# Kernel tuning notes

Hardware: AMD Instinct MI355X
Metric: run time of the kernel (lower is better)

Reference implementation:

```python
import jax, jax.numpy as jnp
import numpy as np

# Expert output sizes per answer type: yes/no, number, other (VQA v2)
SIZES = [2, 482, 3129]
MAX_ANS = max(SIZES)  # 3129, padded output width
D_IN = 1024
D_HID = 1000
BATCH = 16384
N_TYPES = len(SIZES)


def setup_inputs() -> dict:
    key = jax.random.key(0)
    ks = jax.random.split(key, 2 + 4 * N_TYPES)
    inp = {
        "hidden_states": jax.random.normal(ks[0], (BATCH, D_IN), dtype=jnp.float32),
        "question_type_output": jax.random.normal(ks[1], (BATCH, N_TYPES), dtype=jnp.float32),
    }
    # Learned params for each expert MLP: Linear(1024->1000), Tanh, Linear(1000->n_e)
    for e, n_out in enumerate(SIZES):
        k1, k2, k3, k4 = ks[2 + 4 * e], ks[3 + 4 * e], ks[4 + 4 * e], ks[5 + 4 * e]
        inp[f"w1_{e}"] = jax.random.normal(k1, (D_IN, D_HID), dtype=jnp.float32) * 0.02
        inp[f"b1_{e}"] = jax.random.normal(k2, (D_HID,), dtype=jnp.float32) * 0.02
        inp[f"w2_{e}"] = jax.random.normal(k3, (D_HID, n_out), dtype=jnp.float32) * 0.02
        inp[f"b2_{e}"] = jax.random.normal(k4, (n_out,), dtype=jnp.float32) * 0.02
    return inp


def _expert(x, w1, b1, w2, b2):
    # Linear -> Dropout(eval: identity) -> Tanh -> Linear
    return jnp.tanh(x @ w1 + b1) @ w2 + b2


def reference(hidden_states, question_type_output,
              w1_0, b1_0, w2_0, b2_0,
              w1_1, b1_1, w2_1, b2_1,
              w1_2, b1_2, w2_2, b2_2):
    params = [(w1_0, b1_0, w2_0, b2_0),
              (w1_1, b1_1, w2_1, b2_1),
              (w1_2, b1_2, w2_2, b2_2)]
    # Route each sample to the expert of its argmax question type.
    pred = jnp.argmax(question_type_output, axis=1)  # [B] int
    out = jnp.zeros((hidden_states.shape[0], MAX_ANS), dtype=hidden_states.dtype)
    # Small fixed loop over N_TYPES experts (structurally distinct weights);
    # each expert runs batched over all samples, then a mask selects routed rows.
    for e, (w1, b1, w2, b2) in enumerate(params):
        o = _expert(hidden_states, w1, b1, w2, b2)          # [B, n_e]
        o = jnp.pad(o, ((0, 0), (0, MAX_ANS - o.shape[1])))  # zero-pad to [B, MAX]
        out = jnp.where((pred == e)[:, None], o, out)
    return out
```

## Files before the change

### kernel.cpp

```cpp
#include <hip/hip_runtime.h>

typedef __attribute__((ext_vector_type(8))) __bf16 bf16x8;
typedef __attribute__((ext_vector_type(4))) float f32x4;

constexpr int BATCH = 16384;
constexpr int DIN   = 1024;
constexpr int DHID  = 1000;
constexpr int MAXA  = 3129;
constexpr int MBMAX = 131;

constexpr size_t SZ_AP  = (size_t)MBMAX * 32 * 8192;
constexpr size_t SZ_HP  = SZ_AP;
constexpr size_t SZ_W1P = 3 * 8 * 32 * 8192;
constexpr size_t SZ_W2P = 30 * 32 * 8192;
constexpr size_t WS_HP  = 0;
constexpr size_t WS_W1P = WS_HP + SZ_HP;
constexpr size_t WS_W2P = WS_W1P + SZ_W1P;
constexpr size_t WS_CNT = WS_W2P + SZ_W2P;
constexpr size_t WS_IDX = WS_CNT + 64;
constexpr size_t WS_AP  = WS_IDX + 3 * BATCH * 4;
constexpr size_t WS_NEED = WS_AP + SZ_AP;

constexpr int PA_BLK = 2096;
constexpr int PW1_BLK = 1536;
constexpr int PW2_BLK = 1920;

__device__ __forceinline__ ushort f2bf(float f) {
    return __builtin_bit_cast(ushort, (__bf16)f);
}

__device__ __forceinline__ void gload16(const void* g, void* l) {
    __builtin_amdgcn_global_load_lds((const __attribute__((address_space(1))) void*)g,
                                     (__attribute__((address_space(3))) void*)l, 16, 0, 0);
}

__global__ void zero_k(int* __restrict__ c) {
    if (threadIdx.x < 16) c[threadIdx.x] = 0;
}

__global__ void route_k(const float* __restrict__ qt, int* __restrict__ counts,
                        int* __restrict__ idx) {
    int i = blockIdx.x * 256 + threadIdx.x;
    if (i >= BATCH) return;
    float a = qt[3 * i], b = qt[3 * i + 1], c = qt[3 * i + 2];
    int p = 0; float m = a;
    if (b > m) { m = b; p = 1; }
    if (c > m) { m = c; p = 2; }
    int pos = atomicAdd(&counts[p], 1);
    idx[p * BATCH + pos] = i;
}

__global__ void pack_all_k(const float* __restrict__ hs,
                           const float* __restrict__ w1_0, const float* __restrict__ w1_1,
                           const float* __restrict__ w1_2,
                           const float* __restrict__ w2_0, const float* __restrict__ w2_1,
                           const float* __restrict__ w2_2,
                           const int* __restrict__ counts, const int* __restrict__ idx,
                           ushort* __restrict__ Ap, ushort* __restrict__ W1p,
                           ushort* __restrict__ W2p) {
    const int b = blockIdx.x, tid = threadIdx.x;
    if (b < PA_BLK) {
        const int g = b * 256 + tid;
        const int m = g & 127, kt = (g >> 7) & 31, mb = g >> 12;
        const int c0 = counts[0], c1 = counts[1], c2 = counts[2];
        const int n0 = (c0 + 127) >> 7, n1 = (c1 + 127) >> 7, n2 = (c2 + 127) >> 7;
        if (mb >= n0 + n1 + n2) return;
        int e = 0, lm = mb, cnt = c0;
        if (lm >= n0) { lm -= n0; e = 1; cnt = c1; }
        if (e == 1 && lm >= n1) { lm -= n1; e = 2; cnt = c2; }
        int ri = lm * 128 + m; if (ri >= cnt) ri = cnt - 1;
        const float* row = hs + (size_t)idx[e * BATCH + ri] * DIN + kt * 32;
        ushort* dst = Ap + (size_t)(mb * 32 + kt) * 4096 + m * 8;
#pragma unroll
        for (int kc = 0; kc < 4; kc++) {
            float4 f0 = *reinterpret_cast<const float4*>(row + kc * 8);
            float4 f1 = *reinterpret_cast<const float4*>(row + kc * 8 + 4);
            union { ushort u[8]; int4 v; } p;
            p.u[0] = f2bf(f0.x); p.u[1] = f2bf(f0.y); p.u[2] = f2bf(f0.z); p.u[3] = f2bf(f0.w);
            p.u[4] = f2bf(f1.x); p.u[5] = f2bf(f1.y); p.u[6] = f2bf(f1.z); p.u[7] = f2bf(f1.w);
            *reinterpret_cast<int4*>(dst + kc * 1024) = p.v;
        }
    } else if (b < PA_BLK + PW1_BLK) {
        const int g = (b - PA_BLK) * 256 + tid;
        const int n = g & 127, kc = (g >> 7) & 3, kt = (g >> 9) & 31, nb = (g >> 14) & 7, e = g >> 17;
        const float* W = e == 0 ? w1_0 : e == 1 ? w1_1 : w1_2;
        const int nn = nb * 128 + n;
        union { ushort u[8]; int4 v; } p;
#pragma unroll
        for (int j = 0; j < 8; j++) {
            int k = kt * 32 + kc * 8 + j;
            float f = (nn < DHID) ? W[(size_t)k * DHID + nn] : 0.f;
            p.u[j] = f2bf(f);
        }
        *reinterpret_cast<int4*>(W1p + ((size_t)((e * 8 + nb) * 32 + kt)) * 4096 + (kc * 128 + n) * 8) = p.v;
    } else {
        const int g = (b - PA_BLK - PW1_BLK) * 256 + tid;
        const int n = g & 127, kc = (g >> 7) & 3, kt = (g >> 9) & 31, t = g >> 14;
        const int e = (t < 1) ? 0 : (t < 5) ? 1 : 2;
        const int nb = t - (e == 0 ? 0 : e == 1 ? 1 : 5);
        const int ne = e == 0 ? 2 : e == 1 ? 482 : MAXA;
        const float* W = e == 0 ? w2_0 : e == 1 ? w2_1 : w2_2;
        const int nn = nb * 128 + n;
        union { ushort u[8]; int4 v; } p;
#pragma unroll
        for (int j = 0; j < 8; j++) {
            int k = kt * 32 + kc * 8 + j;
            float f = (k < DHID && nn < ne) ? W[(size_t)k * ne + nn] : 0.f;
            p.u[j] = f2bf(f);
        }
        *reinterpret_cast<int4*>(W2p + ((size_t)(t * 32 + kt)) * 4096 + (kc * 128 + n) * 8) = p.v;
    }
}

#define STAGE(BUFO, KT)                                                         \
    {                                                                           \
        const char* as_ = Ag + (size_t)(KT) * 8192 + tid * 16;                  \
        char* ad_ = lds + (BUFO) + w * 1024;                                    \
        gload16(as_, ad_);                                                      \
        gload16(as_ + 4096, ad_ + 4096);                                        \
        const char* bs_ = Bg + (size_t)(KT) * 8192 + tid * 16;                  \
        gload16(bs_, ad_ + 8192);                                               \
        gload16(bs_ + 4096, ad_ + 12288);                                       \
    }

#define KLOOP()                                                                 \
    f32x4 acc[4][4] = {};                                                       \
    STAGE(0, 0)                                                                 \
    STAGE(16384, 1)                                                             \
    {                                                                           \
        int cur = 0;                                                            \
        for (int kt = 0; kt < 32; ++kt) {                                       \
            if (kt < 31) asm volatile("s_waitcnt vmcnt(4)" ::: "memory");       \
            else         asm volatile("s_waitcnt vmcnt(0)" ::: "memory");       \
            asm volatile("s_barrier" ::: "memory");                             \
            if (kt + 2 < 32) {                                                  \
                int nx = cur + 2; if (nx >= 3) nx -= 3;                         \
                STAGE(nx * 16384, kt + 2)                                       \
            }                                                                   \
            const char* base = lds + cur * 16384;                               \
            bf16x8 af[4], bfr[4];                                               \
            _Pragma("unroll")                                                   \
            for (int mi = 0; mi < 4; mi++)                                      \
                af[mi] = *reinterpret_cast<const bf16x8*>(                      \
                    base + kq4 * 2048 + (wm * 64 + mi * 16 + l15) * 16);        \
            _Pragma("unroll")                                                   \
            for (int ni = 0; ni < 4; ni++)                                      \
                bfr[ni] = *reinterpret_cast<const bf16x8*>(                     \
                    base + 8192 + kq4 * 2048 + (wn * 64 + ni * 16 + l15) * 16); \
            __builtin_amdgcn_s_setprio(1);                                      \
            _Pragma("unroll")                                                   \
            for (int mi = 0; mi < 4; mi++)                                      \
                _Pragma("unroll")                                               \
                for (int ni = 0; ni < 4; ni++)                                  \
                    acc[mi][ni] = __builtin_amdgcn_mfma_f32_16x16x32_bf16(      \
                        af[mi], bfr[ni], acc[mi][ni], 0, 0, 0);                 \
            __builtin_amdgcn_s_setprio(0);                                      \
            cur = cur + 1; if (cur == 3) cur = 0;                               \
        }                                                                       \
    }                                                                           \
    asm volatile("s_barrier" ::: "memory");

__global__ __launch_bounds__(256, 3)
void gemm1_k(const char* __restrict__ ApB, const char* __restrict__ W1pB,
             const float* __restrict__ b1_0, const float* __restrict__ b1_1,
             const float* __restrict__ b1_2,
             const int* __restrict__ counts, int* __restrict__ wq,
             char* __restrict__ HpB) {
    __shared__ __align__(16) char lds[49152];
    __shared__ int s_t;
    const int c0 = counts[0], c1 = counts[1], c2 = counts[2];
    const int n0 = (c0 + 127) >> 7, n1 = (c1 + 127) >> 7, n2 = (c2 + 127) >> 7;
    const int T = (n0 + n1 + n2) * 8;

    const int tid = threadIdx.x;
    const int lane = tid & 63, w = tid >> 6, wm = w >> 1, wn = w & 1;
    const int l15 = lane & 15, kq4 = lane >> 4;

    for (;;) {
        if (tid == 0) s_t = atomicAdd(wq, 1);
        __syncthreads();
        const int t = s_t;
        if (t >= T) break;

        const int mbG = t >> 3, nbk = t & 7;
        int e = 0, lm = mbG;
        if (lm >= n0) { lm -= n0; e = 1; }
        if (e == 1 && lm >= n1) { lm -= n1; e = 2; }
        const float* bias = e == 0 ? b1_0 : e == 1 ? b1_1 : b1_2;
        const char* Ag = ApB + (size_t)mbG * (32 * 8192);
        const char* Bg = W1pB + (size_t)((e * 8 + nbk) * 32) * 8192;

        KLOOP()

        ushort* img = (ushort*)lds;
#pragma unroll
        for (int mi = 0; mi < 4; mi++) {
            const int rb = wm * 64 + mi * 16 + kq4 * 4;
#pragma unroll
            for (int ni = 0; ni < 4; ni++) {
                const int nl = wn * 64 + ni * 16 + l15;
                const int ng = nbk * 128 + nl;
                const bool live = ng < DHID;
                const float bv = live ? bias[ng] : 0.f;
                const int ua = ((nl >> 5) * 4096 + ((nl >> 3) & 3) * 1024 + (nl & 6)) & ~1;
#pragma unroll
                for (int rg = 0; rg < 4; rg++) {
                    float vv = live ? tanhf(acc[mi][ni][rg] + bv) : 0.f;
                    float vo = __shfl_xor(vv, 1);
                    ushort lo = (l15 & 1) ? f2bf(vo) : f2bf(vv);
                    ushort hi = (l15 & 1) ? f2bf(vv) : f2bf(vo);
                    *reinterpret_cast<uint*>(img + ua + (rb + rg) * 8) =
                        (uint)lo | ((uint)hi << 16);
                }
            }
        }
        asm volatile("s_barrier" ::: "memory");
        char* hdst = HpB + ((size_t)mbG * 32 + nbk * 4) * 8192;
#pragma unroll
        for (int i2 = 0; i2 < 8; i2++) {
            const int s = tid + i2 * 256;
            *reinterpret_cast<int4*>(hdst + s * 16) =
                *reinterpret_cast<const int4*>(lds + s * 16);
        }
        asm volatile("s_barrier" ::: "memory");
    }
}

__global__ __launch_bounds__(256, 3)
void gemm2_k(const char* __restrict__ HpB, const char* __restrict__ W2pB,
             const float* __restrict__ b2_0, const float* __restrict__ b2_1,
             const float* __restrict__ b2_2,
             const int* __restrict__ counts, const int* __restrict__ idx,
             int* __restrict__ wq, int do_zero, float* __restrict__ Out) {
    __shared__ __align__(16) char lds[49152];
    __shared__ int s_t;
    const int c0 = counts[0], c1 = counts[1], c2 = counts[2];
    int nb[3]  = {(c0 + 127) >> 7, (c1 + 127) >> 7, (c2 + 127) >> 7};
    int cc[3]  = {c0, c1, c2};
    const int nbn[3]  = {1, 4, 25};
    const int nz[3]   = {24, 21, 0};
    const int zst[3]  = {128, 512, 0};
    const int toff[3] = {0, 1, 5};
    const int nel[3]  = {2, 482, MAXA};
    const int Tc = nb[0] * 1 + nb[1] * 4 + nb[2] * 25;
    const int Tz = do_zero ? (nb[0] * 24 + nb[1] * 21) : 0;
    const int T = Tc + Tz;

    const int tid = threadIdx.x;
    const int lane = tid & 63, w = tid >> 6, wm = w >> 1, wn = w & 1;
    const int l15 = lane & 15, kq4 = lane >> 4;

    for (;;) {
        if (tid == 0) s_t = atomicAdd(wq, 1);
        __syncthreads();
        const int t = s_t;
        if (t >= T) break;

        if (t < Tc) {
            int e = 0, r = t, mbG = 0;
            while (e < 2 && r >= nb[e] * nbn[e]) { r -= nb[e] * nbn[e]; mbG += nb[e]; ++e; }
            const int lm = r / nbn[e], nbk = r - lm * nbn[e];
            mbG += lm;
            const int cnt = cc[e], ne = nel[e];
            const float* bias = e == 0 ? b2_0 : e == 1 ? b2_1 : b2_2;
            const char* Ag = HpB + (size_t)mbG * (32 * 8192);
            const char* Bg = W2pB + (size_t)((toff[e] + nbk) * 32) * 8192;

            KLOOP()

            const int m0 = lm * 128;
            float* bf32 = (float*)lds;
            const int* ip = idx + e * BATCH;
#pragma unroll
            for (int h = 0; h < 2; h++) {
                if (wm == h) {
#pragma unroll
                    for (int mi = 0; mi < 4; mi++) {
                        const int rl = mi * 16 + kq4 * 4;
#pragma unroll
                        for (int ni = 0; ni < 4; ni++) {
                            const int nl = wn * 64 + ni * 16 + l15;
                            const int ncol = nbk * 128 + nl;
                            const bool live = ncol < ne;
                            const float bv = live ? bias[ncol] : 0.f;
#pragma unroll
                            for (int rg = 0; rg < 4; rg++)
                                bf32[(rl + rg) * 132 + nl] =
                                    live ? (acc[mi][ni][rg] + bv) : 0.f;
                        }
                    }
                }
                asm volatile("s_barrier" ::: "memory");
#pragma unroll
                for (int i2 = 0; i2 < 8; i2++) {
                    const int s = tid + i2 * 256;
                    const int rr = s >> 5, c4 = s & 31;
                    const int mrow = m0 + h * 64 + rr;
                    const int ncol0 = nbk * 128 + c4 * 4;
                    if (mrow < cnt && ncol0 < ne) {
                        const int orow = ip[mrow];
                        float4 val = *reinterpret_cast<const float4*>(bf32 + rr * 132 + c4 * 4);
                        float* op = Out + (size_t)orow * MAXA + ncol0;
                        if (ncol0 + 3 < MAXA) {
                            *reinterpret_cast<float4*>(op) = val;
                        } else {
                            if (ncol0 + 0 < MAXA) op[0] = val.x;
                            if (ncol0 + 1 < MAXA) op[1] = val.y;
                            if (ncol0 + 2 < MAXA) op[2] = val.z;
                            if (ncol0 + 3 < MAXA) op[3] = val.w;
                        }
                    }
                }
                asm volatile("s_barrier" ::: "memory");
            }
        } else {
            int e = 0, r = t - Tc;
            while (e < 2 && r >= nb[e] * nz[e]) { r -= nb[e] * nz[e]; ++e; }
            const int lm = r / nz[e], zc = r - lm * nz[e];
            const int cnt = cc[e];
            const int col0 = zst[e] + zc * 128;
            const int width = (MAXA - col0 < 128) ? (MAXA - col0) : 128;
            const int m0 = lm * 128;
            const int nrow = (cnt - m0 < 128) ? (cnt - m0) : 128;
            const int* rowp = idx + e * BATCH + m0;
            const float4 z4 = {0.f, 0.f, 0.f, 0.f};
            if (width == 128) {
                for (int s = tid; s < (nrow << 5); s += 256) {
                    const int rl = s >> 5, c4 = s & 31;
                    *reinterpret_cast<float4*>(Out + (size_t)rowp[rl] * MAXA + col0 + c4 * 4) = z4;
                }
            } else {
                const int f4 = width >> 2;
                for (int s = tid; s < nrow * f4; s += 256) {
                    const int rl = s / f4, c4 = s - rl * f4;
                    *reinterpret_cast<float4*>(Out + (size_t)rowp[rl] * MAXA + col0 + c4 * 4) = z4;
                }
                const int rem = width & 3;
                for (int s = tid; s < nrow * rem; s += 256) {
                    const int rl = s / rem, j = s - rl * rem;
                    Out[(size_t)rowp[rl] * MAXA + col0 + f4 * 4 + j] = 0.f;
                }
            }
            __syncthreads();
        }
    }
}

extern "C" void kernel_launch(void* const* d_in, const int* in_sizes, int n_in,
                              void* d_out, int out_size, void* d_ws, size_t ws_size,
                              hipStream_t stream) {
    const float* hs = (const float*)d_in[0];
    const float* qt = (const float*)d_in[1];
    const float* w1_0 = (const float*)d_in[2],  *b1_0 = (const float*)d_in[3];
    const float* w2_0 = (const float*)d_in[4],  *b2_0 = (const float*)d_in[5];
    const float* w1_1 = (const float*)d_in[6],  *b1_1 = (const float*)d_in[7];
    const float* w2_1 = (const float*)d_in[8],  *b2_1 = (const float*)d_in[9];
    const float* w1_2 = (const float*)d_in[10], *b1_2 = (const float*)d_in[11];
    const float* w2_2 = (const float*)d_in[12], *b2_2 = (const float*)d_in[13];

    char* ws = (char*)d_ws;
    ushort* Hp  = (ushort*)(ws + WS_HP);
    ushort* W1p = (ushort*)(ws + WS_W1P);
    ushort* W2p = (ushort*)(ws + WS_W2P);
    int* counts = (int*)(ws + WS_CNT);
    int* idx    = (int*)(ws + WS_IDX);
    const int fallback = (ws_size >= WS_NEED) ? 0 : 1;
    ushort* Ap = fallback ? (ushort*)((char*)d_out + ((size_t)out_size * 4 - SZ_AP))
                          : (ushort*)(ws + WS_AP);
    float* Out = (float*)d_out;

    zero_k<<<1, 64, 0, stream>>>(counts);
    route_k<<<64, 256, 0, stream>>>(qt, counts, idx);
    pack_all_k<<<PA_BLK + PW1_BLK + PW2_BLK, 256, 0, stream>>>(
        hs, w1_0, w1_1, w1_2, w2_0, w2_1, w2_2, counts, idx, Ap, W1p, W2p);
    gemm1_k<<<768, 256, 0, stream>>>((const char*)Ap, (const char*)W1p,
                                     b1_0, b1_1, b1_2, counts, counts + 8, (char*)Hp);
    gemm2_k<<<768, 256, 0, stream>>>((const char*)Hp, (const char*)W2p,
                                     b2_0, b2_1, b2_2, counts, idx, counts + 12,
                                     fallback, Out);
}
```

Baseline: 300.7 us.

## Widen GEMM tiles to 128x256 with repacked weights and wider epilogue

Both GEMM kernels move from 128x128 output tiles to 128x256 tiles. Each wave now holds a 4x8 MFMA accumulator block, so every loaded A fragment is reused across twice as many B columns. Weight packing is reorganised into 256-wide column tiles, LDS per block grows to 72KB, and occupancy drops from 3 to 2 blocks per CU with a smaller persistent grid. The aim is to cut LDS and global traffic per FLOP, at the cost of more register pressure, lower occupancy, and more wasted padded work on the narrow experts.

```diff
diff --git a/kernel.cpp b/kernel.cpp
--- a/kernel.cpp
+++ b/kernel.cpp
@@ -11,19 +11,19 @@
 
 constexpr size_t SZ_AP  = (size_t)MBMAX * 32 * 8192;
 constexpr size_t SZ_HP  = SZ_AP;
-constexpr size_t SZ_W1P = 3 * 8 * 32 * 8192;
-constexpr size_t SZ_W2P = 30 * 32 * 8192;
+constexpr size_t SZ_W1P = (size_t)12 * 32 * 16384;
+constexpr size_t SZ_W2P = (size_t)16 * 32 * 16384;
 constexpr size_t WS_HP  = 0;
 constexpr size_t WS_W1P = WS_HP + SZ_HP;
 constexpr size_t WS_W2P = WS_W1P + SZ_W1P;
 constexpr size_t WS_CNT = WS_W2P + SZ_W2P;
-constexpr size_t WS_IDX = WS_CNT + 64;
-constexpr size_t WS_AP  = WS_IDX + 3 * BATCH * 4;
+constexpr size_t WS_IDX = WS_CNT + 1024;
+constexpr size_t WS_AP  = WS_IDX + (size_t)3 * BATCH * 4;
 constexpr size_t WS_NEED = WS_AP + SZ_AP;
 
-constexpr int PA_BLK = 2096;
-constexpr int PW1_BLK = 1536;
-constexpr int PW2_BLK = 1920;
+constexpr int PA_BLK  = 2096;
+constexpr int PW1_BLK = 384;
+constexpr int PW2_BLK = 512;
 
 __device__ __forceinline__ ushort f2bf(float f) {
     return __builtin_bit_cast(ushort, (__bf16)f);
@@ -34,9 +34,7 @@
                                      (__attribute__((address_space(3))) void*)l, 16, 0, 0);
 }
 
-__global__ void zero_k(int* __restrict__ c) {
-    if (threadIdx.x < 16) c[threadIdx.x] = 0;
-}
+__global__ void zero_k(int* __restrict__ c) { if (threadIdx.x < 16) c[threadIdx.x] = 0; }
 
 __global__ void route_k(const float* __restrict__ qt, int* __restrict__ counts,
                         int* __restrict__ idx) {
@@ -81,77 +79,89 @@
             *reinterpret_cast<int4*>(dst + kc * 1024) = p.v;
         }
     } else if (b < PA_BLK + PW1_BLK) {
-        const int g = (b - PA_BLK) * 256 + tid;
-        const int n = g & 127, kc = (g >> 7) & 3, kt = (g >> 9) & 31, nb = (g >> 14) & 7, e = g >> 17;
+        const int bb = b - PA_BLK;
+        const int kt = bb & 31, tile = bb >> 5;
+        const int e = tile >> 2, nbk = tile & 3;
         const float* W = e == 0 ? w1_0 : e == 1 ? w1_1 : w1_2;
-        const int nn = nb * 128 + n;
-        union { ushort u[8]; int4 v; } p;
-#pragma unroll
-        for (int j = 0; j < 8; j++) {
-            int k = kt * 32 + kc * 8 + j;
-            float f = (nn < DHID) ? W[(size_t)k * DHID + nn] : 0.f;
-            p.u[j] = f2bf(f);
-        }
-        *reinterpret_cast<int4*>(W1p + ((size_t)((e * 8 + nb) * 32 + kt)) * 4096 + (kc * 128 + n) * 8) = p.v;
+        const int n = nbk * 256 + tid;
+        ushort* dst = W1p + (size_t)(tile * 32 + kt) * 8192 + tid * 8;
+#pragma unroll
+        for (int kc = 0; kc < 4; kc++) {
+            union { ushort u[8]; int4 v; } p;
+#pragma unroll
+            for (int j = 0; j < 8; j++) {
+                int k = kt * 32 + kc * 8 + j;
+                float f = (n < DHID) ? W[(size_t)k * DHID + n] : 0.f;
+                p.u[j] = f2bf(f);
+            }
+            *reinterpret_cast<int4*>(dst + kc * 2048) = p.v;
+        }
     } else {
-        const int g = (b - PA_BLK - PW1_BLK) * 256 + tid;
-        const int n = g & 127, kc = (g >> 7) & 3, kt = (g >> 9) & 31, t = g >> 14;
-        const int e = (t < 1) ? 0 : (t < 5) ? 1 : 2;
-        const int nb = t - (e == 0 ? 0 : e == 1 ? 1 : 5);
+        const int bb = b - PA_BLK - PW1_BLK;
+        const int kt = bb & 31, t = bb >> 5;
+        const int e = (t < 1) ? 0 : (t < 3) ? 1 : 2;
+        const int nb = t - (e == 0 ? 0 : e == 1 ? 1 : 3);
         const int ne = e == 0 ? 2 : e == 1 ? 482 : MAXA;
         const float* W = e == 0 ? w2_0 : e == 1 ? w2_1 : w2_2;
-        const int nn = nb * 128 + n;
-        union { ushort u[8]; int4 v; } p;
-#pragma unroll
-        for (int j = 0; j < 8; j++) {
-            int k = kt * 32 + kc * 8 + j;
-            float f = (k < DHID && nn < ne) ? W[(size_t)k * ne + nn] : 0.f;
-            p.u[j] = f2bf(f);
-        }
-        *reinterpret_cast<int4*>(W2p + ((size_t)(t * 32 + kt)) * 4096 + (kc * 128 + n) * 8) = p.v;
+        const int nn = nb * 256 + tid;
+        ushort* dst = W2p + (size_t)(t * 32 + kt) * 8192 + tid * 8;
+#pragma unroll
+        for (int kc = 0; kc < 4; kc++) {
+            union { ushort u[8]; int4 v; } p;
+#pragma unroll
+            for (int j = 0; j < 8; j++) {
+                int k = kt * 32 + kc * 8 + j;
+                float f = (k < DHID && nn < ne) ? W[(size_t)k * ne + nn] : 0.f;
+                p.u[j] = f2bf(f);
+            }
+            *reinterpret_cast<int4*>(dst + kc * 2048) = p.v;
+        }
     }
 }
 
-#define STAGE(BUFO, KT)                                                         \
+#define STAGE6(BUFO, KT)                                                        \
     {                                                                           \
         const char* as_ = Ag + (size_t)(KT) * 8192 + tid * 16;                  \
         char* ad_ = lds + (BUFO) + w * 1024;                                    \
         gload16(as_, ad_);                                                      \
         gload16(as_ + 4096, ad_ + 4096);                                        \
-        const char* bs_ = Bg + (size_t)(KT) * 8192 + tid * 16;                  \
-        gload16(bs_, ad_ + 8192);                                               \
-        gload16(bs_ + 4096, ad_ + 12288);                                       \
+        const char* bs_ = Bg + (size_t)(KT) * 16384 + tid * 16;                 \
+        char* bd_ = lds + (BUFO) + 8192 + w * 1024;                             \
+        gload16(bs_, bd_);                                                      \
+        gload16(bs_ + 4096, bd_ + 4096);                                        \
+        gload16(bs_ + 8192, bd_ + 8192);                                        \
+        gload16(bs_ + 12288, bd_ + 12288);                                      \
     }
 
-#define KLOOP()                                                                 \
-    f32x4 acc[4][4] = {};                                                       \
-    STAGE(0, 0)                                                                 \
-    STAGE(16384, 1)                                                             \
+#define KLOOP256()                                                              \
+    f32x4 acc[4][8] = {};                                                       \
+    STAGE6(0, 0)                                                                \
+    STAGE6(24576, 1)                                                            \
     {                                                                           \
         int cur = 0;                                                            \
         for (int kt = 0; kt < 32; ++kt) {                                       \
-            if (kt < 31) asm volatile("s_waitcnt vmcnt(4)" ::: "memory");       \
+            if (kt < 31) asm volatile("s_waitcnt vmcnt(6)" ::: "memory");       \
             else         asm volatile("s_waitcnt vmcnt(0)" ::: "memory");       \
             asm volatile("s_barrier" ::: "memory");                             \
             if (kt + 2 < 32) {                                                  \
                 int nx = cur + 2; if (nx >= 3) nx -= 3;                         \
-                STAGE(nx * 16384, kt + 2)                                       \
+                STAGE6(nx * 24576, kt + 2)                                      \
             }                                                                   \
-            const char* base = lds + cur * 16384;                               \
-            bf16x8 af[4], bfr[4];                                               \
+            const char* base = lds + cur * 24576;                               \
+            bf16x8 af[4], bfr[8];                                               \
             _Pragma("unroll")                                                   \
             for (int mi = 0; mi < 4; mi++)                                      \
                 af[mi] = *reinterpret_cast<const bf16x8*>(                      \
                     base + kq4 * 2048 + (wm * 64 + mi * 16 + l15) * 16);        \
             _Pragma("unroll")                                                   \
-            for (int ni = 0; ni < 4; ni++)                                      \
+            for (int ni = 0; ni < 8; ni++)                                      \
                 bfr[ni] = *reinterpret_cast<const bf16x8*>(                     \
-                    base + 8192 + kq4 * 2048 + (wn * 64 + ni * 16 + l15) * 16); \
+                    base + 8192 + kq4 * 4096 + (wn * 128 + ni * 16 + l15) * 16);\
             __builtin_amdgcn_s_setprio(1);                                      \
             _Pragma("unroll")                                                   \
             for (int mi = 0; mi < 4; mi++)                                      \
                 _Pragma("unroll")                                               \
-                for (int ni = 0; ni < 4; ni++)                                  \
+                for (int ni = 0; ni < 8; ni++)                                  \
                     acc[mi][ni] = __builtin_amdgcn_mfma_f32_16x16x32_bf16(      \
                         af[mi], bfr[ni], acc[mi][ni], 0, 0, 0);                 \
             __builtin_amdgcn_s_setprio(0);                                      \
@@ -160,17 +170,17 @@
     }                                                                           \
     asm volatile("s_barrier" ::: "memory");
 
-__global__ __launch_bounds__(256, 3)
+__global__ __launch_bounds__(256, 2)
 void gemm1_k(const char* __restrict__ ApB, const char* __restrict__ W1pB,
              const float* __restrict__ b1_0, const float* __restrict__ b1_1,
              const float* __restrict__ b1_2,
              const int* __restrict__ counts, int* __restrict__ wq,
              char* __restrict__ HpB) {
-    __shared__ __align__(16) char lds[49152];
+    __shared__ __align__(16) char lds[73728];
     __shared__ int s_t;
     const int c0 = counts[0], c1 = counts[1], c2 = counts[2];
     const int n0 = (c0 + 127) >> 7, n1 = (c1 + 127) >> 7, n2 = (c2 + 127) >> 7;
-    const int T = (n0 + n1 + n2) * 8;
+    const int T = (n0 + n1 + n2) * 4;
 
     const int tid = threadIdx.x;
     const int lane = tid & 63, w = tid >> 6, wm = w >> 1, wn = w & 1;
@@ -182,27 +192,27 @@
         const int t = s_t;
         if (t >= T) break;
 
-        const int mbG = t >> 3, nbk = t & 7;
+        const int mbG = t >> 2, nbk = t & 3;
         int e = 0, lm = mbG;
         if (lm >= n0) { lm -= n0; e = 1; }
         if (e == 1 && lm >= n1) { lm -= n1; e = 2; }
         const float* bias = e == 0 ? b1_0 : e == 1 ? b1_1 : b1_2;
         const char* Ag = ApB + (size_t)mbG * (32 * 8192);
-        const char* Bg = W1pB + (size_t)((e * 8 + nbk) * 32) * 8192;
-
-        KLOOP()
+        const char* Bg = W1pB + (size_t)((e * 4 + nbk) * 32) * 16384;
+
+        KLOOP256()
 
         ushort* img = (ushort*)lds;
 #pragma unroll
         for (int mi = 0; mi < 4; mi++) {
             const int rb = wm * 64 + mi * 16 + kq4 * 4;
 #pragma unroll
-            for (int ni = 0; ni < 4; ni++) {
-                const int nl = wn * 64 + ni * 16 + l15;
-                const int ng = nbk * 128 + nl;
+            for (int ni = 0; ni < 8; ni++) {
+                const int nl = wn * 128 + ni * 16 + l15;
+                const int ng = nbk * 256 + nl;
                 const bool live = ng < DHID;
                 const float bv = live ? bias[ng] : 0.f;
-                const int ua = ((nl >> 5) * 4096 + ((nl >> 3) & 3) * 1024 + (nl & 6)) & ~1;
+                const int ua = (nl >> 5) * 4096 + ((nl >> 3) & 3) * 1024 + (nl & 6);
 #pragma unroll
                 for (int rg = 0; rg < 4; rg++) {
                     float vv = live ? tanhf(acc[mi][ni][rg] + bv) : 0.f;
@@ -215,9 +225,9 @@
             }
         }
         asm volatile("s_barrier" ::: "memory");
-        char* hdst = HpB + ((size_t)mbG * 32 + nbk * 4) * 8192;
-#pragma unroll
-        for (int i2 = 0; i2 < 8; i2++) {
+        char* hdst = HpB + ((size_t)mbG * 32 + nbk * 8) * 8192;
+#pragma unroll
+        for (int i2 = 0; i2 < 16; i2++) {
             const int s = tid + i2 * 256;
             *reinterpret_cast<int4*>(hdst + s * 16) =
                 *reinterpret_cast<const int4*>(lds + s * 16);
@@ -226,24 +236,24 @@
     }
 }
 
-__global__ __launch_bounds__(256, 3)
+__global__ __launch_bounds__(256, 2)
 void gemm2_k(const char* __restrict__ HpB, const char* __restrict__ W2pB,
              const float* __restrict__ b2_0, const float* __restrict__ b2_1,
              const float* __restrict__ b2_2,
              const int* __restrict__ counts, const int* __restrict__ idx,
-             int* __restrict__ wq, int do_zero, float* __restrict__ Out) {
-    __shared__ __align__(16) char lds[49152];
+             int* __restrict__ wq, int fallback, float* __restrict__ Out) {
+    __shared__ __align__(16) char lds[73728];
     __shared__ int s_t;
     const int c0 = counts[0], c1 = counts[1], c2 = counts[2];
     int nb[3]  = {(c0 + 127) >> 7, (c1 + 127) >> 7, (c2 + 127) >> 7};
     int cc[3]  = {c0, c1, c2};
-    const int nbn[3]  = {1, 4, 25};
-    const int nz[3]   = {24, 21, 0};
-    const int zst[3]  = {128, 512, 0};
-    const int toff[3] = {0, 1, 5};
+    const int nbn[3]  = {1, 2, 13};
+    const int nz[3]   = {23, 21, 0};
+    const int zst[3]  = {256, 512, 0};
+    const int toff[3] = {0, 1, 3};
     const int nel[3]  = {2, 482, MAXA};
-    const int Tc = nb[0] * 1 + nb[1] * 4 + nb[2] * 25;
-    const int Tz = do_zero ? (nb[0] * 24 + nb[1] * 21) : 0;
+    const int Tc = nb[0] * 1 + nb[1] * 2 + nb[2] * 13;
+    const int Tz = fallback ? (nb[0] * 23 + nb[1] * 21) : 0;
     const int T = Tc + Tz;
 
     const int tid = threadIdx.x;
@@ -264,9 +274,9 @@
             const int cnt = cc[e], ne = nel[e];
             const float* bias = e == 0 ? b2_0 : e == 1 ? b2_1 : b2_2;
             const char* Ag = HpB + (size_t)mbG * (32 * 8192);
-            const char* Bg = W2pB + (size_t)((toff[e] + nbk) * 32) * 8192;
-
-            KLOOP()
+            const char* Bg = W2pB + (size_t)((toff[e] + nbk) * 32) * 16384;
+
+            KLOOP256()
 
             const int m0 = lm * 128;
             float* bf32 = (float*)lds;
@@ -278,28 +288,28 @@
                     for (int mi = 0; mi < 4; mi++) {
                         const int rl = mi * 16 + kq4 * 4;
 #pragma unroll
-                        for (int ni = 0; ni < 4; ni++) {
-                            const int nl = wn * 64 + ni * 16 + l15;
-                            const int ncol = nbk * 128 + nl;
+                        for (int ni = 0; ni < 8; ni++) {
+                            const int nl = wn * 128 + ni * 16 + l15;
+                            const int ncol = nbk * 256 + nl;
                             const bool live = ncol < ne;
                             const float bv = live ? bias[ncol] : 0.f;
 #pragma unroll
                             for (int rg = 0; rg < 4; rg++)
-                                bf32[(rl + rg) * 132 + nl] =
+                                bf32[(rl + rg) * 260 + nl] =
                                     live ? (acc[mi][ni][rg] + bv) : 0.f;
                         }
                     }
                 }
                 asm volatile("s_barrier" ::: "memory");
 #pragma unroll
-                for (int i2 = 0; i2 < 8; i2++) {
+                for (int i2 = 0; i2 < 16; i2++) {
                     const int s = tid + i2 * 256;
-                    const int rr = s >> 5, c4 = s & 31;
+                    const int rr = s >> 6, c4 = s & 63;
                     const int mrow = m0 + h * 64 + rr;
-                    const int ncol0 = nbk * 128 + c4 * 4;
-                    if (mrow < cnt && ncol0 < ne) {
+                    const int ncol0 = nbk * 256 + c4 * 4;
+                    if (mrow < cnt && ncol0 < MAXA && (ncol0 < ne || fallback)) {
                         const int orow = ip[mrow];
-                        float4 val = *reinterpret_cast<const float4*>(bf32 + rr * 132 + c4 * 4);
+                        float4 val = *reinterpret_cast<const float4*>(bf32 + rr * 260 + c4 * 4);
                         float* op = Out + (size_t)orow * MAXA + ncol0;
                         if (ncol0 + 3 < MAXA) {
                             *reinterpret_cast<float4*>(op) = val;
@@ -307,7 +317,6 @@
                             if (ncol0 + 0 < MAXA) op[0] = val.x;
                             if (ncol0 + 1 < MAXA) op[1] = val.y;
                             if (ncol0 + 2 < MAXA) op[2] = val.z;
-                            if (ncol0 + 3 < MAXA) op[3] = val.w;
                         }
                     }
                 }
@@ -373,9 +382,9 @@
     route_k<<<64, 256, 0, stream>>>(qt, counts, idx);
     pack_all_k<<<PA_BLK + PW1_BLK + PW2_BLK, 256, 0, stream>>>(
         hs, w1_0, w1_1, w1_2, w2_0, w2_1, w2_2, counts, idx, Ap, W1p, W2p);
-    gemm1_k<<<768, 256, 0, stream>>>((const char*)Ap, (const char*)W1p,
+    gemm1_k<<<512, 256, 0, stream>>>((const char*)Ap, (const char*)W1p,
                                      b1_0, b1_1, b1_2, counts, counts + 8, (char*)Hp);
-    gemm2_k<<<768, 256, 0, stream>>>((const char*)Hp, (const char*)W2p,
+    gemm2_k<<<512, 256, 0, stream>>>((const char*)Hp, (const char*)W2p,
                                      b2_0, b2_1, b2_2, counts, idx, counts + 12,
                                      fallback, Out);
 }
```

After: 349.0 us. +16.1%, slower.
